# Kernel tuning notes

Hardware: AMD Instinct MI355X
Metric: run time of the kernel (lower is better)

## Reference

```python
import jax, jax.numpy as jnp
import numpy as np

EDGE_LABELS = jnp.arange(5, dtype=jnp.float32)  # possible ratings 0..4
NUM_USERS, NUM_MOVIES, HIDDEN, NUM_EDGES = 100000, 50000, 64, 1000000


def setup_inputs() -> dict:
    key = jax.random.key(0)
    k1, k2, k3, k4 = jax.random.split(key, 4)
    z_user = jax.random.normal(k1, (NUM_USERS, HIDDEN), dtype=jnp.float32)
    z_movie = jax.random.normal(k2, (NUM_MOVIES, HIDDEN), dtype=jnp.float32)
    rel_emb = jax.random.normal(k3, (EDGE_LABELS.shape[0], HIDDEN), dtype=jnp.float32)
    edge_label_index = jax.random.randint(k4, (2, NUM_EDGES), 0, NUM_MOVIES, dtype=jnp.int64)
    return {"z_user": z_user, "z_movie": z_movie, "rel_emb": rel_emb,
            "edge_label_index": edge_label_index}


def reference(z_user, z_movie, rel_emb, edge_label_index):
    # Gather endpoint embeddings once: [E, H]
    z_src = z_user[edge_label_index[0]]
    z_dst = z_movie[edge_label_index[1]]
    # Per-relation bilinear score: sum_h z_src*rel_r*z_dst -> [E, R]
    scores = jnp.einsum('eh,rh->er', z_src * z_dst, rel_emb)
    probs = jax.nn.softmax(scores, axis=1)
    # Expected rating under softmax distribution: [E]
    predicted_ratings = probs @ EDGE_LABELS
    return predicted_ratings
```

## Files before the change

### kernel.cpp

```cpp
#include <hip/hip_runtime.h>
#include <hip/hip_fp16.h>

#define H 64
#define R 5

typedef float    v2f __attribute__((ext_vector_type(2)));
typedef _Float16 v2h __attribute__((ext_vector_type(2)));

static __device__ __forceinline__ v2f fma2(v2f a, v2f b, v2f c) {
#if __has_builtin(__builtin_elementwise_fma)
    return __builtin_elementwise_fma(a, b, c);
#else
    return a * b + c;
#endif
}

static __device__ __forceinline__ float dot2(v2h a, v2h b, float c) {
#if __has_builtin(__builtin_amdgcn_fdot2)
    return __builtin_amdgcn_fdot2(a, b, c, false);
#else
    return (float)a.x * (float)b.x + (float)a.y * (float)b.y + c;
#endif
}

static __device__ __forceinline__ v2h bch(unsigned u) {
    return __builtin_bit_cast(v2h, u);
}

static __device__ __forceinline__ unsigned h2pair(float a, float b) {
    __half2 h = __floats2half2_rn(a, b);
    return *(const unsigned*)&h;
}

__global__ __launch_bounds__(256) void convert_f16_kernel(
    const float4* __restrict__ zu4, const float4* __restrict__ zm4,
    const float4* __restrict__ rel4,
    uint4* __restrict__ wu, uint4* __restrict__ wm, uint4* __restrict__ wr,
    int n_u_chunks, int n_m_chunks, int n_r_chunks)
{
    int t = blockIdx.x * blockDim.x + threadIdx.x;
    const float4* src;
    uint4* dst;
    int c;
    if (t < n_u_chunks)                   { src = zu4;  dst = wu; c = t; }
    else if (t < n_u_chunks + n_m_chunks) { src = zm4;  dst = wm; c = t - n_u_chunks; }
    else if (t < n_u_chunks + n_m_chunks + n_r_chunks)
                                          { src = rel4; dst = wr; c = t - n_u_chunks - n_m_chunks; }
    else return;
    float4 f0 = src[2 * c];
    float4 f1 = src[2 * c + 1];
    uint4 o;
    o.x = h2pair(f0.x, f0.y);
    o.y = h2pair(f0.z, f0.w);
    o.z = h2pair(f1.x, f1.y);
    o.w = h2pair(f1.z, f1.w);
    dst[c] = o;
}

__global__ __launch_bounds__(256) void edge_decoder_f16o_kernel(
    const uint4* __restrict__ wu,
    const uint4* __restrict__ wm,
    const uint4* __restrict__ wr,
    const int*   __restrict__ idx,
    float*       __restrict__ out,
    int E)
{
    int tid  = blockIdx.x * blockDim.x + threadIdx.x;
    int l    = tid & 7;
    int base = tid & ~7;
    if (base >= E) return;

    int su_l = 0, sm_l = 0;
    if (tid < E) { su_l = idx[tid]; sm_l = idx[E + tid]; }

    int su0 = __shfl(su_l, 0, 8);
    int su1 = __shfl(su_l, 1, 8);
    int su2 = __shfl(su_l, 2, 8);
    int su3 = __shfl(su_l, 3, 8);
    int su4 = __shfl(su_l, 4, 8);
    int su5 = __shfl(su_l, 5, 8);
    int su6 = __shfl(su_l, 6, 8);
    int su7 = __shfl(su_l, 7, 8);
    int sm0 = __shfl(sm_l, 0, 8);
    int sm1 = __shfl(sm_l, 1, 8);
    int sm2 = __shfl(sm_l, 2, 8);
    int sm3 = __shfl(sm_l, 3, 8);
    int sm4 = __shfl(sm_l, 4, 8);
    int sm5 = __shfl(sm_l, 5, 8);
    int sm6 = __shfl(sm_l, 6, 8);
    int sm7 = __shfl(sm_l, 7, 8);

#define ROWS(j)                                          \
    uint4 a_##j = wu[(size_t)su##j * 8 + l];             \
    uint4 b_##j = wm[(size_t)sm##j * 8 + l];
    ROWS(0) ROWS(1) ROWS(2) ROWS(3) ROWS(4) ROWS(5) ROWS(6) ROWS(7)
#undef ROWS

#define RELS(r)                                          \
    uint4 w_##r = wr[r * 8 + l];
    RELS(0) RELS(1) RELS(2) RELS(3) RELS(4)
#undef RELS

#define MAKE_P(j)                                        \
    v2h p##j##_0 = bch(a_##j.x) * bch(b_##j.x);          \
    v2h p##j##_1 = bch(a_##j.y) * bch(b_##j.y);          \
    v2h p##j##_2 = bch(a_##j.z) * bch(b_##j.z);          \
    v2h p##j##_3 = bch(a_##j.w) * bch(b_##j.w);
    MAKE_P(0) MAKE_P(1) MAKE_P(2) MAKE_P(3)
    MAKE_P(4) MAKE_P(5) MAKE_P(6) MAKE_P(7)
#undef MAKE_P

    bool c1 = (l & 1) != 0;
    bool c2 = (l & 2) != 0;
    bool c4 = (l & 4) != 0;

#define SCORE(j, r)                                                   \
    dot2(p##j##_3, bch(w_##r.w), dot2(p##j##_2, bch(w_##r.z),         \
    dot2(p##j##_1, bch(w_##r.y), dot2(p##j##_0, bch(w_##r.x), 0.f))))

    float sc0, sc1, sc2, sc3, sc4;
#define REDUCE(r, scr) {                                                   \
        float s0 = SCORE(0, r); float s1 = SCORE(1, r);                    \
        float s2 = SCORE(2, r); float s3 = SCORE(3, r);                    \
        float s4 = SCORE(4, r); float s5 = SCORE(5, r);                    \
        float s6 = SCORE(6, r); float s7 = SCORE(7, r);                    \
        float m01 = c1 ? s1 : s0, o01 = c1 ? s0 : s1;                      \
        float m23 = c1 ? s3 : s2, o23 = c1 ? s2 : s3;                      \
        float m45 = c1 ? s5 : s4, o45 = c1 ? s4 : s5;                      \
        float m67 = c1 ? s7 : s6, o67 = c1 ? s6 : s7;                      \
        m01 += __shfl_xor(o01, 1); m23 += __shfl_xor(o23, 1);              \
        m45 += __shfl_xor(o45, 1); m67 += __shfl_xor(o67, 1);              \
        float n03 = c2 ? m23 : m01, q03 = c2 ? m01 : m23;                  \
        float n47 = c2 ? m67 : m45, q47 = c2 ? m45 : m67;                  \
        n03 += __shfl_xor(q03, 2); n47 += __shfl_xor(q47, 2);              \
        float fv  = c4 ? n47 : n03, qf  = c4 ? n03 : n47;                  \
        fv += __shfl_xor(qf, 4);                                           \
        scr = fv;                                                          \
    }
    REDUCE(0, sc0) REDUCE(1, sc1) REDUCE(2, sc2) REDUCE(3, sc3) REDUCE(4, sc4)
#undef REDUCE
#undef SCORE

    float mx = fmaxf(fmaxf(fmaxf(sc0, sc1), fmaxf(sc2, sc3)), sc4);
    float e0 = __expf(sc0 - mx);
    float e1 = __expf(sc1 - mx);
    float e2 = __expf(sc2 - mx);
    float e3 = __expf(sc3 - mx);
    float e4 = __expf(sc4 - mx);
    float den = e0 + e1 + e2 + e3 + e4;
    float num = fmaf(4.f, e4, fmaf(3.f, e3, fmaf(2.f, e2, e1)));
    if (tid < E) out[tid] = num * __frcp_rn(den);
}

__global__ __launch_bounds__(256) void edge_decoder_f32_kernel(
    const float4* __restrict__ zu4, const float4* __restrict__ zm4,
    const float4* __restrict__ rel4, const int* __restrict__ idx,
    float* __restrict__ out, int E)
{
    int tid = blockIdx.x * blockDim.x + threadIdx.x;
    int l   = threadIdx.x & 3;
    int e   = tid >> 2;
    if (e >= E) return;
    int su = idx[e];
    int sm = idx[E + e];
    const float4* arow = zu4 + su * 16;
    const float4* brow = zm4 + sm * 16;
    v2f plo[4], phi[4];
#pragma unroll
    for (int i = 0; i < 4; ++i) {
        float4 av = arow[4 * i + l];
        float4 bv = brow[4 * i + l];
        v2f alo = {av.x, av.y}, ahi = {av.z, av.w};
        v2f blo = {bv.x, bv.y}, bhi = {bv.z, bv.w};
        plo[i] = alo * blo;
        phi[i] = ahi * bhi;
    }
    float s[R];
#pragma unroll
    for (int r = 0; r < R; ++r) {
        v2f acc = {0.f, 0.f};
#pragma unroll
        for (int i = 0; i < 4; ++i) {
            float4 w = rel4[r * 16 + 4 * i + l];
            acc = fma2(plo[i], (v2f){w.x, w.y}, acc);
            acc = fma2(phi[i], (v2f){w.z, w.w}, acc);
        }
        s[r] = acc.x + acc.y;
    }
#pragma unroll
    for (int r = 0; r < R; ++r) s[r] += __shfl_xor(s[r], 1);
#pragma unroll
    for (int r = 0; r < R; ++r) s[r] += __shfl_xor(s[r], 2);
    if (l == 0) {
        float mx = fmaxf(fmaxf(fmaxf(s[0], s[1]), fmaxf(s[2], s[3])), s[4]);
        float e0 = __expf(s[0] - mx);
        float e1 = __expf(s[1] - mx);
        float e2 = __expf(s[2] - mx);
        float e3 = __expf(s[3] - mx);
        float e4 = __expf(s[4] - mx);
        float den = e0 + e1 + e2 + e3 + e4;
        float num = fmaf(4.f, e4, fmaf(3.f, e3, fmaf(2.f, e2, e1)));
        out[e] = num * __frcp_rn(den);
    }
}

extern "C" void kernel_launch(void* const* d_in, const int* in_sizes, int n_in,
                              void* d_out, int out_size, void* d_ws, size_t ws_size,
                              hipStream_t stream) {
    const float4* zu4  = (const float4*)d_in[0];
    const float4* zm4  = (const float4*)d_in[1];
    const float4* rel4 = (const float4*)d_in[2];
    const int*    idx  = (const int*)d_in[3];
    float* out = (float*)d_out;

    int E  = in_sizes[3] / 2;
    int nu = in_sizes[0] / H;
    int nm = in_sizes[1] / H;

    size_t need = (size_t)(nu + nm + R) * H * 2;
    int block = 256;

    if (ws_size >= need) {
        uint4* wu = (uint4*)d_ws;
        uint4* wm = wu + (size_t)nu * 8;
        uint4* wr = wm + (size_t)nm * 8;

        int n_u_chunks = nu * (H / 8);
        int n_m_chunks = nm * (H / 8);
        int n_r_chunks = R * (H / 8);
        int conv_threads = n_u_chunks + n_m_chunks + n_r_chunks;
        int conv_grid = (conv_threads + block - 1) / block;
        convert_f16_kernel<<<conv_grid, block, 0, stream>>>(
            zu4, zm4, rel4, wu, wm, wr, n_u_chunks, n_m_chunks, n_r_chunks);

        long long threads = (long long)E;
        int grid = (int)((threads + block - 1) / block);
        edge_decoder_f16o_kernel<<<grid, block, 0, stream>>>(
            wu, wm, wr, idx, out, E);
    } else {
        long long threads = (long long)E * 4;
        int grid = (int)((threads + block - 1) / block);
        edge_decoder_f32_kernel<<<grid, block, 0, stream>>>(
            zu4, zm4, rel4, idx, out, E);
    }
}
```

Measured before the change: 115.2 us.

## Drop fp16 conversion pass and gather fp32 rows directly in decoder

Removes the pre-pass that converted the user, movie and relation tables to fp16 in workspace, and the fp32 fallback kernel. The decoder now loads fp32 rows directly as two float4 per lane and computes the bilinear scores with packed fp32 FMAs. This avoids reading and rewriting the whole tables each call and saves one launch. In exchange each gathered row is twice as large and register pressure grows.

Result: slower. 138.6 us (+20.3%).

```diff
diff --git a/kernel.cpp b/kernel.cpp
--- a/kernel.cpp
+++ b/kernel.cpp
@@ -1,11 +1,9 @@
 #include <hip/hip_runtime.h>
-#include <hip/hip_fp16.h>
 
 #define H 64
 #define R 5
 
-typedef float    v2f __attribute__((ext_vector_type(2)));
-typedef _Float16 v2h __attribute__((ext_vector_type(2)));
+typedef float v2f __attribute__((ext_vector_type(2)));
 
 static __device__ __forceinline__ v2f fma2(v2f a, v2f b, v2f c) {
 #if __has_builtin(__builtin_elementwise_fma)
@@ -15,52 +13,10 @@
 #endif
 }
 
-static __device__ __forceinline__ float dot2(v2h a, v2h b, float c) {
-#if __has_builtin(__builtin_amdgcn_fdot2)
-    return __builtin_amdgcn_fdot2(a, b, c, false);
-#else
-    return (float)a.x * (float)b.x + (float)a.y * (float)b.y + c;
-#endif
-}
-
-static __device__ __forceinline__ v2h bch(unsigned u) {
-    return __builtin_bit_cast(v2h, u);
-}
-
-static __device__ __forceinline__ unsigned h2pair(float a, float b) {
-    __half2 h = __floats2half2_rn(a, b);
-    return *(const unsigned*)&h;
-}
-
-__global__ __launch_bounds__(256) void convert_f16_kernel(
-    const float4* __restrict__ zu4, const float4* __restrict__ zm4,
+__global__ __launch_bounds__(256) void edge_decoder_f32o_kernel(
+    const float4* __restrict__ zu4,
+    const float4* __restrict__ zm4,
     const float4* __restrict__ rel4,
-    uint4* __restrict__ wu, uint4* __restrict__ wm, uint4* __restrict__ wr,
-    int n_u_chunks, int n_m_chunks, int n_r_chunks)
-{
-    int t = blockIdx.x * blockDim.x + threadIdx.x;
-    const float4* src;
-    uint4* dst;
-    int c;
-    if (t < n_u_chunks)                   { src = zu4;  dst = wu; c = t; }
-    else if (t < n_u_chunks + n_m_chunks) { src = zm4;  dst = wm; c = t - n_u_chunks; }
-    else if (t < n_u_chunks + n_m_chunks + n_r_chunks)
-                                          { src = rel4; dst = wr; c = t - n_u_chunks - n_m_chunks; }
-    else return;
-    float4 f0 = src[2 * c];
-    float4 f1 = src[2 * c + 1];
-    uint4 o;
-    o.x = h2pair(f0.x, f0.y);
-    o.y = h2pair(f0.z, f0.w);
-    o.z = h2pair(f1.x, f1.y);
-    o.w = h2pair(f1.z, f1.w);
-    dst[c] = o;
-}
-
-__global__ __launch_bounds__(256) void edge_decoder_f16o_kernel(
-    const uint4* __restrict__ wu,
-    const uint4* __restrict__ wm,
-    const uint4* __restrict__ wr,
     const int*   __restrict__ idx,
     float*       __restrict__ out,
     int E)
@@ -90,33 +46,41 @@
     int sm6 = __shfl(sm_l, 6, 8);
     int sm7 = __shfl(sm_l, 7, 8);
 
-#define ROWS(j)                                          \
-    uint4 a_##j = wu[(size_t)su##j * 8 + l];             \
-    uint4 b_##j = wm[(size_t)sm##j * 8 + l];
-    ROWS(0) ROWS(1) ROWS(2) ROWS(3) ROWS(4) ROWS(5) ROWS(6) ROWS(7)
-#undef ROWS
-
-#define RELS(r)                                          \
-    uint4 w_##r = wr[r * 8 + l];
+#define RELS(r)                                  \
+    float4 w0_##r = rel4[r * 16 + l];            \
+    float4 w1_##r = rel4[r * 16 + 8 + l];
     RELS(0) RELS(1) RELS(2) RELS(3) RELS(4)
 #undef RELS
 
-#define MAKE_P(j)                                        \
-    v2h p##j##_0 = bch(a_##j.x) * bch(b_##j.x);          \
-    v2h p##j##_1 = bch(a_##j.y) * bch(b_##j.y);          \
-    v2h p##j##_2 = bch(a_##j.z) * bch(b_##j.z);          \
-    v2h p##j##_3 = bch(a_##j.w) * bch(b_##j.w);
+#define ROWS(j)                                          \
+    float4 a0_##j = zu4[(size_t)su##j * 16 + l];         \
+    float4 a1_##j = zu4[(size_t)su##j * 16 + 8 + l];     \
+    float4 b0_##j = zm4[(size_t)sm##j * 16 + l];         \
+    float4 b1_##j = zm4[(size_t)sm##j * 16 + 8 + l];
+
+#define MAKE_P(j)                                                       \
+    v2f p##j##_0 = (v2f){a0_##j.x, a0_##j.y} * (v2f){b0_##j.x, b0_##j.y}; \
+    v2f p##j##_1 = (v2f){a0_##j.z, a0_##j.w} * (v2f){b0_##j.z, b0_##j.w}; \
+    v2f p##j##_2 = (v2f){a1_##j.x, a1_##j.y} * (v2f){b1_##j.x, b1_##j.y}; \
+    v2f p##j##_3 = (v2f){a1_##j.z, a1_##j.w} * (v2f){b1_##j.z, b1_##j.w};
+
+    ROWS(0) ROWS(1) ROWS(2) ROWS(3)
     MAKE_P(0) MAKE_P(1) MAKE_P(2) MAKE_P(3)
+    ROWS(4) ROWS(5) ROWS(6) ROWS(7)
     MAKE_P(4) MAKE_P(5) MAKE_P(6) MAKE_P(7)
 #undef MAKE_P
+#undef ROWS
 
     bool c1 = (l & 1) != 0;
     bool c2 = (l & 2) != 0;
     bool c4 = (l & 4) != 0;
 
-#define SCORE(j, r)                                                   \
-    dot2(p##j##_3, bch(w_##r.w), dot2(p##j##_2, bch(w_##r.z),         \
-    dot2(p##j##_1, bch(w_##r.y), dot2(p##j##_0, bch(w_##r.x), 0.f))))
+#define SCORE(j, r) ({                                            \
+        v2f acc_ = p##j##_0 * (v2f){w0_##r.x, w0_##r.y};          \
+        acc_ = fma2(p##j##_1, (v2f){w0_##r.z, w0_##r.w}, acc_);   \
+        acc_ = fma2(p##j##_2, (v2f){w1_##r.x, w1_##r.y}, acc_);   \
+        acc_ = fma2(p##j##_3, (v2f){w1_##r.z, w1_##r.w}, acc_);   \
+        acc_.x + acc_.y; })
 
     float sc0, sc1, sc2, sc3, sc4;
 #define REDUCE(r, scr) {                                                   \
@@ -152,58 +116,6 @@
     if (tid < E) out[tid] = num * __frcp_rn(den);
 }
 
-__global__ __launch_bounds__(256) void edge_decoder_f32_kernel(
-    const float4* __restrict__ zu4, const float4* __restrict__ zm4,
-    const float4* __restrict__ rel4, const int* __restrict__ idx,
-    float* __restrict__ out, int E)
-{
-    int tid = blockIdx.x * blockDim.x + threadIdx.x;
-    int l   = threadIdx.x & 3;
-    int e   = tid >> 2;
-    if (e >= E) return;
-    int su = idx[e];
-    int sm = idx[E + e];
-    const float4* arow = zu4 + su * 16;
-    const float4* brow = zm4 + sm * 16;
-    v2f plo[4], phi[4];
-#pragma unroll
-    for (int i = 0; i < 4; ++i) {
-        float4 av = arow[4 * i + l];
-        float4 bv = brow[4 * i + l];
-        v2f alo = {av.x, av.y}, ahi = {av.z, av.w};
-        v2f blo = {bv.x, bv.y}, bhi = {bv.z, bv.w};
-        plo[i] = alo * blo;
-        phi[i] = ahi * bhi;
-    }
-    float s[R];
-#pragma unroll
-    for (int r = 0; r < R; ++r) {
-        v2f acc = {0.f, 0.f};
-#pragma unroll
-        for (int i = 0; i < 4; ++i) {
-            float4 w = rel4[r * 16 + 4 * i + l];
-            acc = fma2(plo[i], (v2f){w.x, w.y}, acc);
-            acc = fma2(phi[i], (v2f){w.z, w.w}, acc);
-        }
-        s[r] = acc.x + acc.y;
-    }
-#pragma unroll
-    for (int r = 0; r < R; ++r) s[r] += __shfl_xor(s[r], 1);
-#pragma unroll
-    for (int r = 0; r < R; ++r) s[r] += __shfl_xor(s[r], 2);
-    if (l == 0) {
-        float mx = fmaxf(fmaxf(fmaxf(s[0], s[1]), fmaxf(s[2], s[3])), s[4]);
-        float e0 = __expf(s[0] - mx);
-        float e1 = __expf(s[1] - mx);
-        float e2 = __expf(s[2] - mx);
-        float e3 = __expf(s[3] - mx);
-        float e4 = __expf(s[4] - mx);
-        float den = e0 + e1 + e2 + e3 + e4;
-        float num = fmaf(4.f, e4, fmaf(3.f, e3, fmaf(2.f, e2, e1)));
-        out[e] = num * __frcp_rn(den);
-    }
-}
-
 extern "C" void kernel_launch(void* const* d_in, const int* in_sizes, int n_in,
                               void* d_out, int out_size, void* d_ws, size_t ws_size,
                               hipStream_t stream) {
@@ -213,34 +125,13 @@
     const int*    idx  = (const int*)d_in[3];
     float* out = (float*)d_out;
 
-    int E  = in_sizes[3] / 2;
-    int nu = in_sizes[0] / H;
-    int nm = in_sizes[1] / H;
+    int E = in_sizes[3] / 2;
 
-    size_t need = (size_t)(nu + nm + R) * H * 2;
+    (void)d_ws; (void)ws_size;
+
     int block = 256;
-
-    if (ws_size >= need) {
-        uint4* wu = (uint4*)d_ws;
-        uint4* wm = wu + (size_t)nu * 8;
-        uint4* wr = wm + (size_t)nm * 8;
-
-        int n_u_chunks = nu * (H / 8);
-        int n_m_chunks = nm * (H / 8);
-        int n_r_chunks = R * (H / 8);
-        int conv_threads = n_u_chunks + n_m_chunks + n_r_chunks;
-        int conv_grid = (conv_threads + block - 1) / block;
-        convert_f16_kernel<<<conv_grid, block, 0, stream>>>(
-            zu4, zm4, rel4, wu, wm, wr, n_u_chunks, n_m_chunks, n_r_chunks);
-
-        long long threads = (long long)E;
-        int grid = (int)((threads + block - 1) / block);
-        edge_decoder_f16o_kernel<<<grid, block, 0, stream>>>(
-            wu, wm, wr, idx, out, E);
-    } else {
-        long long threads = (long long)E * 4;
-        int grid = (int)((threads + block - 1) / block);
-        edge_decoder_f32_kernel<<<grid, block, 0, stream>>>(
-            zu4, zm4, rel4, idx, out, E);
-    }
+    long long threads = (long long)E;
+    int grid = (int)((threads + block - 1) / block);
+    edge_decoder_f32o_kernel<<<grid, block, 0, stream>>>(
+        zu4, zm4, rel4, idx, out, E);
 }
```
